# Kernel optimization log

Hardware: AMD Instinct MI355X
Metric: run time of the kernel (lower is better)

The kernel has to match this reference:

```python
import jax, jax.numpy as jnp
import numpy as np

N_STATES = 256
N_FEATURES = 32000
SEQ_LEN = 8192


def setup_inputs() -> dict:
    key = jax.random.key(0)
    k1, k2, k3, k4 = jax.random.split(key, 4)
    startprob = jax.random.uniform(k1, (N_STATES,), dtype=jnp.float32)
    startprob = startprob / startprob.sum()
    transmat = jax.random.uniform(k2, (N_STATES, N_STATES), dtype=jnp.float32)
    transmat = transmat / transmat.sum(axis=1, keepdims=True)
    emissionprob = jax.random.uniform(k3, (N_STATES, N_FEATURES), dtype=jnp.float32)
    emissionprob = emissionprob / emissionprob.sum(axis=1, keepdims=True)
    obs = jax.random.randint(k4, (SEQ_LEN,), 0, N_FEATURES, dtype=jnp.int64)
    return {"startprob": startprob, "transmat": transmat,
            "emissionprob": emissionprob, "obs": obs}


def reference(startprob, transmat, emissionprob, obs):
    """HMM forward algorithm (order-1, log-space).

    Returns alpha of shape (n_states, T) where
    alpha[i, t] = log P(O_1..O_t, q_t = S_i | theta).
    """
    log_start = jnp.log(startprob)                # [N]
    log_A = jnp.log(transmat)                     # [N, N]
    log_E = jnp.log(emissionprob)                 # [N, V]
    log_e_obs = log_E[:, obs].T                   # [T, N] gathered emissions

    alpha0 = log_start + log_e_obs[0]             # [N]

    def step(prev, log_e_t):
        # logsumexp over source state i: prev[i] + log_A[i, j]
        a = jax.nn.logsumexp(prev[:, None] + log_A, axis=0) + log_e_t
        return a, a

    _, alphas = jax.lax.scan(step, alpha0, log_e_obs[1:])   # [T-1, N]
    alpha = jnp.concatenate([alpha0[None, :], alphas], axis=0)  # [T, N]
    return alpha.T                                 # [N, T]
```

## Files before the change

### kernel.cpp

```cpp
#include <hip/hip_runtime.h>
#include <hip/hip_bf16.h>
#include <math.h>

#define NS 256
#define T_LEN 8192
#define NF 32000
#define L_CH 8
#define B_BN 8
#define S_TOT 16
#define C_CH 1024
#define G_CH 16
#define NBLK 64
#define SCALE 32768.0f
#define XPAD 264
#define TCHUNK 512

typedef short short8 __attribute__((ext_vector_type(8)));
typedef float f32x4 __attribute__((ext_vector_type(4)));

__device__ __forceinline__ short f2bs(float f) {
    union { __bf16 b; short s; } u; u.b = (__bf16)f; return u.s;
}
__device__ __forceinline__ float bs2f(short s) {
    union { short s; __bf16 b; } u; u.s = s; return (float)u.b;
}

__device__ __forceinline__ void sync_lds_only() {
    __builtin_amdgcn_sched_barrier(0);
    asm volatile("s_waitcnt lgkmcnt(0)" ::: "memory");
    __builtin_amdgcn_s_barrier();
    __builtin_amdgcn_sched_barrier(0);
}

__global__ __launch_bounds__(256)
void prep(const float* __restrict__ E, const int* __restrict__ obs,
          const float* __restrict__ A,
          float* __restrict__ SE, short* __restrict__ Aswz) {
    const int bid = blockIdx.x;
    if (bid < 256) {
        const int jg = bid & 15, tc = bid >> 4;
        const int t0 = tc * TCHUNK;
        __shared__ int olds[TCHUNK];
        for (int i = threadIdx.x; i < TCHUNK; i += 256)
            olds[i] = obs[t0 + i];
        __syncthreads();
        const int jl = threadIdx.x & 15;
        const int tl = threadIdx.x >> 4;
        const int j  = jg * 16 + jl;
        const float* Erow = E + (size_t)j * NF;
#pragma unroll 4
        for (int p = 0; p < TCHUNK / 16; ++p) {
            int t_loc = p * 16 + tl;
            int o = olds[t_loc];
            SE[(size_t)(t0 + t_loc) * NS + j] = Erow[o] * SCALE;
        }
    } else if (bid < 288) {
        const int pb   = (bid - 256) * 4 + (threadIdx.x >> 6);
        const int lane = threadIdx.x & 63;
        const int ntg  = pb >> 3;
        const int kk   = pb & 7;
        const int col  = ntg * 16 + (lane & 15);
        const int krow = kk * 32 + (lane >> 4) * 8;
        short8 v;
#pragma unroll
        for (int e = 0; e < 8; ++e)
            v[e] = f2bs(A[(size_t)(krow + e) * NS + col]);
        *(short8*)&Aswz[((size_t)pb * 64 + lane) * 8] = v;
    }
}

__global__ __launch_bounds__(1024, 4)
void hmm_chains(const float* __restrict__ start,
                const float* __restrict__ SE,
                const short* __restrict__ Aswz,
                unsigned short* __restrict__ zbuf,
                float* __restrict__ Pb, float* __restrict__ Qb)
{
    const int bid  = blockIdx.x;
    const int tid  = threadIdx.x;
    const int wv   = tid >> 6;
    const int lane = tid & 63;
    const int cj   = lane & 15;
    const int rq   = lane >> 4;
    const int col  = wv * 16 + cj;
    const int base = 128 * bid - B_BN;

    __shared__ unsigned short xb[2][G_CH][XPAD];

    short8 bfr[8];
    const short8* Av = (const short8*)Aswz;
#pragma unroll
    for (int kk = 0; kk < 8; ++kk)
        bfr[kk] = Av[((size_t)(wv * 8 + kk)) * 64 + lane];
#pragma unroll
    for (int kk = 0; kk < 8; ++kk)
        asm volatile("" : "+v"(bfr[kk]));

    for (int idx = tid; idx < G_CH * XPAD; idx += 1024)
        ((unsigned short*)xb[0])[idx] = 0x3F80;

    float evc[4], evn[4];
#pragma unroll
    for (int r = 0; r < 4; ++r) {
        int t = base + 8 * (rq * 4 + r) + 1;
        t = t < 0 ? 0 : t;
        evc[r] = SE[(size_t)t * NS + col];
    }

    for (int s = 1; s < S_TOT; ++s) {
        sync_lds_only();
        const int rb = (s - 1) & 1, wb = s & 1;

        if (s == B_BN && tid < 256) {
            int g = tid >> 4, part = tid & 15;
            float ss = 0.f;
            const unsigned short* row = &xb[rb][g][part * 16];
#pragma unroll
            for (int i = 0; i < 16; ++i) ss += bs2f(row[i]);
#pragma unroll
            for (int m = 1; m < 16; m <<= 1) ss += __shfl_xor(ss, m, 16);
            if (part == 0) Qb[bid * G_CH + g] = log2f(ss);
        }

#pragma unroll
        for (int r = 0; r < 4; ++r) {
            int t = base + 8 * (rq * 4 + r) + s + 1;
            t = t < 0 ? 0 : (t > T_LEN - 1 ? T_LEN - 1 : t);
            evn[r] = SE[(size_t)t * NS + col];
        }

        short8 ax[8];
#pragma unroll
        for (int kk = 0; kk < 8; ++kk)
            ax[kk] = *(const short8*)&xb[rb][cj][kk * 32 + rq * 8];

        f32x4 acc = (f32x4){0.f, 0.f, 0.f, 0.f};
#pragma unroll
        for (int kk = 0; kk < 8; ++kk)
            acc = __builtin_amdgcn_mfma_f32_16x16x32_bf16(ax[kk], bfr[kk], acc, 0, 0, 0);

        const bool body = (s >= B_BN);
#pragma unroll
        for (int r = 0; r < 4; ++r) {
            int g = rq * 4 + r;
            float y = acc[r] * evc[r];
            bool skip = (bid == 0) && (s == B_BN) && (g == 0);
            if (!skip) {
                unsigned short yb = (unsigned short)f2bs(y);
                xb[wb][g][col] = yb;
                if (body) {
                    int tg = base + 8 * g + s;
                    zbuf[(size_t)tg * NS + col] = yb;
                }
            }
        }

        if (bid == 0 && s == B_BN && tid < 256) {
            float y0 = start[tid] * SE[tid];
            unsigned short yb = (unsigned short)f2bs(y0);
            xb[wb][0][tid] = yb;
            zbuf[tid] = yb;
        }

#pragma unroll
        for (int r = 0; r < 4; ++r) evc[r] = evn[r];
    }

    sync_lds_only();
    if (tid < 256) {
        int g = tid >> 4, part = tid & 15;
        float ss = 0.f;
        const unsigned short* row = &xb[1][g][part * 16];
#pragma unroll
        for (int i = 0; i < 16; ++i) ss += bs2f(row[i]);
#pragma unroll
        for (int m = 1; m < 16; m <<= 1) ss += __shfl_xor(ss, m, 16);
        if (part == 0) Pb[bid * G_CH + g] = log2f(ss);
    }
}

__global__ __launch_bounds__(1024)
void hmm_stitch(const float* __restrict__ Pb,
                const float* __restrict__ Qb,
                float* __restrict__ Dfull)
{
    __shared__ double x[C_CH];
    const int i = threadIdx.x;
    x[i] = (i == 0) ? 0.0 : ((double)Pb[i - 1] - (double)Qb[i]);
    __syncthreads();
    for (int ofs = 1; ofs < C_CH; ofs <<= 1) {
        double v = (i >= ofs) ? x[i - ofs] : 0.0;
        __syncthreads();
        x[i] += v;
        __syncthreads();
    }
    for (int t = i; t < T_LEN; t += 1024)
        Dfull[t] = (float)(x[t >> 3] - 15.0 * (double)(t + 1));
}

__global__ __launch_bounds__(256)
void hmm_finalize(const unsigned short* __restrict__ zbuf,
                  const float* __restrict__ Dfull,
                  float* __restrict__ out)
{
    __shared__ float tile[64][65];
    const int t0   = blockIdx.x * 64;
    const int j0   = blockIdx.y * 64;
    const int lane = threadIdx.x & 63;
    const int row4 = threadIdx.x >> 6;
    const float LN2 = 0.69314718055994530942f;

#pragma unroll
    for (int r = 0; r < 16; ++r) {
        int trow = r * 4 + row4;
        int t = t0 + trow;
        float z = bs2f((short)zbuf[(size_t)t * NS + j0 + lane]);
        tile[trow][lane] = __log2f(z) + Dfull[t];
    }
    __syncthreads();
#pragma unroll
    for (int r = 0; r < 16; ++r) {
        int jrow = r * 4 + row4;
        out[(size_t)(j0 + jrow) * T_LEN + t0 + lane] = LN2 * tile[lane][jrow];
    }
}

__global__ __launch_bounds__(NS, 1)
void hmm_forward_seq(const float* __restrict__ start,
                     const float* __restrict__ A,
                     const float* __restrict__ E,
                     const int* __restrict__ obs,
                     float* __restrict__ out)
{
    __shared__ float xbuf[2][NS];
    __shared__ float red[4];
    const int j = threadIdx.x;
    float a[NS];
#pragma unroll
    for (int i = 0; i < NS; ++i) a[i] = A[i * NS + j];
    const float LN2 = 0.69314718055994530942f;
    float Eacc = 0.0f;
    float z = start[j] * E[(size_t)j * NF + obs[0]] * SCALE;
    out[(size_t)j * T_LEN + 0] = LN2 * (__log2f(z) - 15.0f);
    xbuf[0][j] = z;
    __syncthreads();
    float se_cur = E[(size_t)j * NF + obs[1]] * SCALE;
    for (int t = 1; t < T_LEN; ++t) {
        float se_nxt = 0.0f;
        if (t + 1 < T_LEN) se_nxt = E[(size_t)j * NF + obs[t + 1]] * SCALE;
        const float4* x4 = (const float4*)xbuf[(t - 1) & 1];
        float y0 = 0.f, y1 = 0.f, y2 = 0.f, y3 = 0.f;
#pragma unroll
        for (int i = 0; i < NS / 4; ++i) {
            float4 xv = x4[i];
            y0 = fmaf(xv.x, a[4 * i + 0], y0);
            y1 = fmaf(xv.y, a[4 * i + 1], y1);
            y2 = fmaf(xv.z, a[4 * i + 2], y2);
            y3 = fmaf(xv.w, a[4 * i + 3], y3);
        }
        float y = ((y0 + y1) + (y2 + y3)) * se_cur;
        se_cur = se_nxt;
        out[(size_t)j * T_LEN + t] =
            LN2 * (__log2f(y) + Eacc - 15.0f * (float)(t + 1));
        float* wr = xbuf[t & 1];
        wr[j] = y;
        __syncthreads();
        if ((t & 1023) == 1023) {
            float v = wr[j];
#pragma unroll
            for (int d = 1; d < 64; d <<= 1) v = fmaxf(v, __shfl_xor(v, d, 64));
            if ((j & 63) == 0) red[j >> 6] = v;
            __syncthreads();
            float m = fmaxf(fmaxf(red[0], red[1]), fmaxf(red[2], red[3]));
            int k = ilogbf(m);
            wr[j] = ldexpf(wr[j], -k);
            Eacc += (float)k;
            __syncthreads();
        }
    }
}

extern "C" void kernel_launch(void* const* d_in, const int* in_sizes, int n_in,
                              void* d_out, int out_size, void* d_ws, size_t ws_size,
                              hipStream_t stream) {
    const float* start = (const float*)d_in[0];
    const float* A     = (const float*)d_in[1];
    const float* E     = (const float*)d_in[2];
    const int*   obs   = (const int*)d_in[3];
    float* out = (float*)d_out;

    char* ws = (char*)d_ws;
    const size_t zb_bytes  = (size_t)T_LEN * NS * sizeof(unsigned short);
    const size_t se_bytes  = (size_t)T_LEN * NS * sizeof(float);
    const size_t asw_bytes = (size_t)128 * 64 * 8 * sizeof(short);

    unsigned short* z = (unsigned short*)ws;
    float* SE    = (float*)(ws + zb_bytes);
    short* Aswz  = (short*)(ws + zb_bytes + se_bytes);
    float* Pb    = (float*)(ws + zb_bytes + se_bytes + asw_bytes);
    float* Qb    = Pb + C_CH;
    float* Dfull = Qb + C_CH;

    const size_t need = zb_bytes + se_bytes + asw_bytes +
                        (2 * C_CH + T_LEN) * sizeof(float);

    if (ws_size >= need) {
        prep<<<288, 256, 0, stream>>>(E, obs, A, SE, Aswz);
        hmm_chains<<<NBLK, 1024, 0, stream>>>(start, SE, Aswz, z, Pb, Qb);
        hmm_stitch<<<1, 1024, 0, stream>>>(Pb, Qb, Dfull);
        hmm_finalize<<<dim3(T_LEN / 64, NS / 64), 256, 0, stream>>>(z, Dfull, out);
    } else {
        hmm_forward_seq<<<1, NS, 0, stream>>>(start, A, E, obs, out);
    }
}
```

Before: 42.58 us.

## Shorten chain length to 2 and use 256 blocks with bf16 emission buffer

The time axis is split into 4096 chains of length 2 instead of 1024 chains of length 8, spread over 256 blocks, so each block runs 9 steps instead of 15. This cuts the serial MFMA step count and fills more compute units. The gathered emission buffer is stored in bf16 to halve its traffic, and the stitch scan now does a 4-per-thread local prefix before the block scan to handle the larger chain count. The bf16 emissions add rounding error, and more chains mean more burn-in recomputation in total.

```diff
diff --git a/kernel.cpp b/kernel.cpp
--- a/kernel.cpp
+++ b/kernel.cpp
@@ -5,12 +5,12 @@
 #define NS 256
 #define T_LEN 8192
 #define NF 32000
-#define L_CH 8
+#define L_CH 2
 #define B_BN 8
-#define S_TOT 16
-#define C_CH 1024
+#define S_TOT 10
+#define C_CH 4096
 #define G_CH 16
-#define NBLK 64
+#define NBLK 256
 #define SCALE 32768.0f
 #define XPAD 264
 #define TCHUNK 512
@@ -35,7 +35,7 @@
 __global__ __launch_bounds__(256)
 void prep(const float* __restrict__ E, const int* __restrict__ obs,
           const float* __restrict__ A,
-          float* __restrict__ SE, short* __restrict__ Aswz) {
+          unsigned short* __restrict__ SEb, short* __restrict__ Aswz) {
     const int bid = blockIdx.x;
     if (bid < 256) {
         const int jg = bid & 15, tc = bid >> 4;
@@ -52,7 +52,8 @@
         for (int p = 0; p < TCHUNK / 16; ++p) {
             int t_loc = p * 16 + tl;
             int o = olds[t_loc];
-            SE[(size_t)(t0 + t_loc) * NS + j] = Erow[o] * SCALE;
+            SEb[(size_t)(t0 + t_loc) * NS + j] =
+                (unsigned short)f2bs(Erow[o] * SCALE);
         }
     } else if (bid < 288) {
         const int pb   = (bid - 256) * 4 + (threadIdx.x >> 6);
@@ -71,7 +72,7 @@
 
 __global__ __launch_bounds__(1024, 4)
 void hmm_chains(const float* __restrict__ start,
-                const float* __restrict__ SE,
+                const unsigned short* __restrict__ SEb,
                 const short* __restrict__ Aswz,
                 unsigned short* __restrict__ zbuf,
                 float* __restrict__ Pb, float* __restrict__ Qb)
@@ -83,7 +84,7 @@
     const int cj   = lane & 15;
     const int rq   = lane >> 4;
     const int col  = wv * 16 + cj;
-    const int base = 128 * bid - B_BN;
+    const int base = 32 * bid - B_BN;
 
     __shared__ unsigned short xb[2][G_CH][XPAD];
 
@@ -102,9 +103,9 @@
     float evc[4], evn[4];
 #pragma unroll
     for (int r = 0; r < 4; ++r) {
-        int t = base + 8 * (rq * 4 + r) + 1;
+        int t = base + 2 * (rq * 4 + r) + 1;
         t = t < 0 ? 0 : t;
-        evc[r] = SE[(size_t)t * NS + col];
+        evc[r] = bs2f((short)SEb[(size_t)t * NS + col]);
     }
 
     for (int s = 1; s < S_TOT; ++s) {
@@ -124,9 +125,9 @@
 
 #pragma unroll
         for (int r = 0; r < 4; ++r) {
-            int t = base + 8 * (rq * 4 + r) + s + 1;
+            int t = base + 2 * (rq * 4 + r) + s + 1;
             t = t < 0 ? 0 : (t > T_LEN - 1 ? T_LEN - 1 : t);
-            evn[r] = SE[(size_t)t * NS + col];
+            evn[r] = bs2f((short)SEb[(size_t)t * NS + col]);
         }
 
         short8 ax[8];
@@ -149,14 +150,14 @@
                 unsigned short yb = (unsigned short)f2bs(y);
                 xb[wb][g][col] = yb;
                 if (body) {
-                    int tg = base + 8 * g + s;
+                    int tg = base + 2 * g + s;
                     zbuf[(size_t)tg * NS + col] = yb;
                 }
             }
         }
 
         if (bid == 0 && s == B_BN && tid < 256) {
-            float y0 = start[tid] * SE[tid];
+            float y0 = start[tid] * bs2f((short)SEb[tid]);
             unsigned short yb = (unsigned short)f2bs(y0);
             xb[wb][0][tid] = yb;
             zbuf[tid] = yb;
@@ -184,18 +185,33 @@
                 const float* __restrict__ Qb,
                 float* __restrict__ Dfull)
 {
-    __shared__ double x[C_CH];
-    const int i = threadIdx.x;
-    x[i] = (i == 0) ? 0.0 : ((double)Pb[i - 1] - (double)Qb[i]);
+    __shared__ double xs[1024];
+    const int tid = threadIdx.x;
+    double loc[4];
+    double s = 0.0;
+#pragma unroll
+    for (int i = 0; i < 4; ++i) {
+        int cc = tid * 4 + i;
+        double d = (cc == 0) ? 0.0 : ((double)Pb[cc - 1] - (double)Qb[cc]);
+        s += d;
+        loc[i] = s;
+    }
+    xs[tid] = s;
     __syncthreads();
-    for (int ofs = 1; ofs < C_CH; ofs <<= 1) {
-        double v = (i >= ofs) ? x[i - ofs] : 0.0;
+    for (int ofs = 1; ofs < 1024; ofs <<= 1) {
+        double v = (tid >= ofs) ? xs[tid - ofs] : 0.0;
         __syncthreads();
-        x[i] += v;
+        xs[tid] += v;
         __syncthreads();
     }
-    for (int t = i; t < T_LEN; t += 1024)
-        Dfull[t] = (float)(x[t >> 3] - 15.0 * (double)(t + 1));
+    const double off = xs[tid] - s;
+#pragma unroll
+    for (int i = 0; i < 4; ++i) {
+        double D = off + loc[i];
+        int t0 = (tid * 4 + i) * 2;
+        Dfull[t0]     = (float)(D - 15.0 * (double)(t0 + 1));
+        Dfull[t0 + 1] = (float)(D - 15.0 * (double)(t0 + 2));
+    }
 }
 
 __global__ __launch_bounds__(256)
@@ -291,11 +307,11 @@
 
     char* ws = (char*)d_ws;
     const size_t zb_bytes  = (size_t)T_LEN * NS * sizeof(unsigned short);
-    const size_t se_bytes  = (size_t)T_LEN * NS * sizeof(float);
+    const size_t se_bytes  = (size_t)T_LEN * NS * sizeof(unsigned short);
     const size_t asw_bytes = (size_t)128 * 64 * 8 * sizeof(short);
 
-    unsigned short* z = (unsigned short*)ws;
-    float* SE    = (float*)(ws + zb_bytes);
+    unsigned short* z   = (unsigned short*)ws;
+    unsigned short* SEb = (unsigned short*)(ws + zb_bytes);
     short* Aswz  = (short*)(ws + zb_bytes + se_bytes);
     float* Pb    = (float*)(ws + zb_bytes + se_bytes + asw_bytes);
     float* Qb    = Pb + C_CH;
@@ -305,8 +321,8 @@
                         (2 * C_CH + T_LEN) * sizeof(float);
 
     if (ws_size >= need) {
-        prep<<<288, 256, 0, stream>>>(E, obs, A, SE, Aswz);
-        hmm_chains<<<NBLK, 1024, 0, stream>>>(start, SE, Aswz, z, Pb, Qb);
+        prep<<<288, 256, 0, stream>>>(E, obs, A, SEb, Aswz);
+        hmm_chains<<<NBLK, 1024, 0, stream>>>(start, SEb, Aswz, z, Pb, Qb);
         hmm_stitch<<<1, 1024, 0, stream>>>(Pb, Qb, Dfull);
         hmm_finalize<<<dim3(T_LEN / 64, NS / 64), 256, 0, stream>>>(z, Dfull, out);
     } else {
```

Result: faster. 37.95 us (-10.9%).
